# Kernel tuning notes

Hardware: AMD Instinct MI355X
Metric: run time of the kernel (lower is better)

## Reference

```python
import jax, jax.numpy as jnp
import numpy as np

HEADS = 8
DIM = 64      # dim
DH = 64       # dim_head
DK = 24       # dim_k (== dim_head_k * heads, required by reshape in forward)
DHK = 3       # dim_head_k (also conv groups)


def setup_inputs() -> dict:
    key = jax.random.key(0)
    ks = jax.random.split(key, 10)
    b, h, w = 4, 128, 128
    return {
        "x_in": jax.random.normal(ks[0], (b, h, w, DIM), jnp.float32),
        "illu_fea_trans": jax.random.normal(ks[1], (b, h, w, DIM), jnp.float32),
        "illu_map_trans": jax.random.normal(ks[2], (b, h, w, DK), jnp.float32),
        # Linear weights stored as [in, out] (torch stores [out, in]; math y = x @ W_in_out)
        "Wq": jax.random.normal(ks[3], (DIM, HEADS * DH), jnp.float32) * 0.05,
        "Wk": jax.random.normal(ks[4], (DK, HEADS * DHK), jnp.float32) * 0.05,
        "Wv": jax.random.normal(ks[5], (DIM, HEADS * DH), jnp.float32) * 0.05,
        "rescale": jnp.ones((HEADS, 1, 1), jnp.float32),
        "Wp": jax.random.normal(ks[6], (HEADS * DHK, DK), jnp.float32) * 0.05,
        "bp": jax.random.normal(ks[7], (DK,), jnp.float32) * 0.05,
        # grouped conv weights, OIHW: [out=24, in/groups=8, 3, 3]
        "conv1_w": jax.random.normal(ks[8], (DK, DK // DHK, 3, 3), jnp.float32) * 0.05,
        "conv2_w": jax.random.normal(ks[9], (DK, DK // DHK, 3, 3), jnp.float32) * 0.05,
    }


def _gconv(x_nchw, w_oihw):
    return jax.lax.conv_general_dilated(
        x_nchw, w_oihw, window_strides=(1, 1), padding='SAME',
        feature_group_count=DHK,
        dimension_numbers=('NCHW', 'OIHW', 'NCHW'))


def reference(x_in, illu_fea_trans, illu_map_trans, Wq, Wk, Wv, rescale, Wp, bp, conv1_w, conv2_w):
    b, h, w, c = x_in.shape
    n = h * w
    # projections
    q = (x_in.reshape(b, n, c) @ Wq).reshape(b, n, HEADS, DH)
    k_inp = illu_map_trans.reshape(b, n, DK) @ Wk            # [b, n, heads*dhk]
    v = (illu_fea_trans.reshape(b, n, c) @ Wv).reshape(b, n, HEADS, DH)
    kh = k_inp.reshape(b, n, HEADS, DHK)
    q = q / (DIM ** 0.5)  # note: scaled by sqrt(dim), not sqrt(dim_head)
    # channel-wise cross-attention: attn over channel dims, contracting tokens n
    attn = jnp.einsum('bnhk,bnhd->bhkd', kh, q) * rescale[None]  # [b, heads, dhk, dh]
    attn = jax.nn.softmax(attn, axis=-1)
    out = jnp.einsum('bhkd,bnhd->bnkh', attn, v)             # [b, n, dhk, heads]
    out = out.reshape(b, n, DHK * HEADS) @ Wp + bp           # proj
    out = out.reshape(b, h, w, DK)
    # positional branch: two grouped 3x3 convs with exact GELU on k_inp
    kx = k_inp.reshape(b, h, w, DK).transpose(0, 3, 1, 2)    # NCHW
    y = _gconv(kx, conv1_w)
    y = jax.nn.gelu(y, approximate=False)
    y = _gconv(y, conv2_w)
    return out + y.transpose(0, 2, 3, 1)
```

## Files before the change

kernel.cpp:

```cpp
#include <hip/hip_runtime.h>
#include <math.h>

#define HEADS 8
#define DIM   64
#define DK    24
#define DHK   3
#define BB    4
#define HH    128
#define WW    128
#define NN    (HH*WW)
#define QSCALE 0.125f

__global__ __launch_bounds__(1024) void s_reduce(
    const float* __restrict__ imap,
    const float* __restrict__ x,
    float* __restrict__ Sp_part,
    float* __restrict__ Pt)
{
    __shared__ float part[16 * 1540];
    const int tid = threadIdx.x;
    const int blk = blockIdx.x;
    const int b = blk >> 6, chunk = blk & 63;
    const int w = tid >> 6, lane = tid & 63;
    const int cq = lane & 15;
    const int ig = lane >> 4;

    const long tok0 = (long)b * NN + chunk * 256 + w * 16;
    const float* xp = x    + tok0 * 64 + cq * 4;
    const float* mp = imap + tok0 * 24 + ig * 6;

    float acc[6][4];
    #pragma unroll
    for (int r = 0; r < 6; ++r)
        #pragma unroll
        for (int q = 0; q < 4; ++q) acc[r][q] = 0.f;

    #pragma unroll 4
    for (int t = 0; t < 16; ++t) {
        float4 xv = *(const float4*)(xp + t * 64);
        float2 m0 = *(const float2*)(mp + t * 24);
        float2 m1 = *(const float2*)(mp + t * 24 + 2);
        float2 m2 = *(const float2*)(mp + t * 24 + 4);
        float mm[6] = {m0.x, m0.y, m1.x, m1.y, m2.x, m2.y};
        #pragma unroll
        for (int r = 0; r < 6; ++r) {
            acc[r][0] += mm[r] * xv.x;
            acc[r][1] += mm[r] * xv.y;
            acc[r][2] += mm[r] * xv.z;
            acc[r][3] += mm[r] * xv.w;
        }
    }

    float* pp = part + w * 1540;
    #pragma unroll
    for (int r = 0; r < 6; ++r) {
        float4 v = {acc[r][0], acc[r][1], acc[r][2], acc[r][3]};
        *(float4*)(pp + (ig * 6 + r) * 64 + cq * 4) = v;
    }
    __syncthreads();

    for (int e = tid; e < 1536; e += 1024) {
        float s = 0.f;
        #pragma unroll
        for (int ww = 0; ww < 16; ++ww) s += part[ww * 1540 + e];
        Sp_part[(long)blk * 1536 + e] = s;
    }
    if (blk < 4)
        for (int e = tid; e < 1536; e += 1024) Pt[blk * 1536 + e] = 0.f;
}

__global__ __launch_bounds__(256) void attn_fused(
    const float* __restrict__ Sp_part,
    const float* __restrict__ Wk,
    const float* __restrict__ Wq,
    const float* __restrict__ Wv,
    const float* __restrict__ rescale,
    const float* __restrict__ Wp,
    float* __restrict__ Pt)
{
    __shared__ float Sp_l[1536];
    __shared__ float sS[192];
    __shared__ float sP[192];
    __shared__ float Wv_l[64 * 65];

    const int tid = threadIdx.x, blk = blockIdx.x;
    const int b = blk >> 3, h = blk & 7;
    const int w = tid >> 6, lane = tid & 63;

    {
        float s[6] = {0.f, 0.f, 0.f, 0.f, 0.f, 0.f};
        const float* p = Sp_part + (long)(b * 64) * 1536 + tid;
        #pragma unroll 8
        for (int pb = 0; pb < 64; ++pb)
            #pragma unroll
            for (int k = 0; k < 6; ++k)
                s[k] += p[(long)pb * 1536 + k * 256];
        #pragma unroll
        for (int k = 0; k < 6; ++k) Sp_l[tid + k * 256] = s[k];
    }
    for (int e = tid; e < 4096; e += 256) {
        int c = e >> 6, d = e & 63;
        Wv_l[c * 65 + d] = Wv[c * 512 + h * 64 + d];
    }
    __syncthreads();

    if (w < 3) {
        const float* wk = Wk + (h * 3 + w);
        float s = 0.f;
        #pragma unroll
        for (int i = 0; i < 24; ++i) s += wk[i * 24] * Sp_l[i * 64 + lane];
        sS[w * 64 + lane] = s;
    }
    __syncthreads();

    if (w < 3) {
        const float* wq = Wq + h * 64 + lane;
        const float* sr = sS + w * 64;
        float a = 0.f;
        #pragma unroll 8
        for (int c = 0; c < 64; ++c) a += sr[c] * wq[c * 512];
        a *= QSCALE * rescale[h];
        float mx = a;
        #pragma unroll
        for (int off = 32; off >= 1; off >>= 1)
            mx = fmaxf(mx, __shfl_xor(mx, off, 64));
        float e = expf(a - mx);
        float sum = e;
        #pragma unroll
        for (int off = 32; off >= 1; off >>= 1)
            sum += __shfl_xor(sum, off, 64);
        sP[w * 64 + lane] = e / sum;
    }
    __syncthreads();

    if (w < 3) {
        const float* pr = sP + w * 64;
        const float* wv = Wv_l + lane * 65;
        float m = 0.f;
        #pragma unroll
        for (int d = 0; d < 64; ++d) m += pr[d] * wv[d];
        sS[w * 64 + lane] = m;
    }
    __syncthreads();

    for (int q = tid; q < 1536; q += 256) {
        int o = q >> 6, c = q & 63;
        float v = 0.f;
        #pragma unroll
        for (int k = 0; k < 3; ++k)
            v += sS[k * 64 + c] * Wp[(k * 8 + h) * 24 + o];
        atomicAdd(&Pt[b * 1536 + o * 64 + c], v);
    }
}

__global__ __launch_bounds__(192, 2) void conv_fused(
    const float* __restrict__ imap, const float* __restrict__ Wk,
    const float* __restrict__ c1w,  const float* __restrict__ fea,
    const float* __restrict__ c2w,  const float* __restrict__ Pt,
    const float* __restrict__ bp,   float* __restrict__ outp)
{
    __shared__ __align__(16) float smem[8784];
    float* kbuf = smem;
    float* feat = smem;
    float* y1l  = smem + 4352;
    float* ptl  = smem + 7152;

    const int tid = threadIdx.x;
    const int blk = blockIdx.x;
    const int b = blk >> 8, ti = (blk >> 4) & 15, tj = blk & 15;
    const int i0 = ti * 8, j0 = tj * 8;
    const int o = tid % 24, jj = tid / 24;
    const int g = o >> 3;

    if (tid < 144) {
        const int pi = tid / 12, pj = tid % 12;
        const int gi = i0 + pi - 2, gj = j0 + pj - 2;
        float kv[24];
        #pragma unroll
        for (int j = 0; j < 24; ++j) kv[j] = 0.f;
        if (gi >= 0 && gi < HH && gj >= 0 && gj < WW) {
            const float4* m4 = (const float4*)(imap + (((long)b * HH + gi) * WW + gj) * 24);
            float m[24];
            #pragma unroll
            for (int i = 0; i < 6; ++i) {
                float4 v = m4[i];
                m[4*i+0]=v.x; m[4*i+1]=v.y; m[4*i+2]=v.z; m[4*i+3]=v.w;
            }
            for (int i = 0; i < 24; ++i) {
                float mi = m[i];
                #pragma unroll
                for (int j = 0; j < 24; ++j) kv[j] += mi * Wk[i * 24 + j];
            }
        }
        #pragma unroll
        for (int j = 0; j < 24; ++j) kbuf[tid * 28 + j] = kv[j];
    }
    __syncthreads();

    {
        float wr[8][9];
        {
            const float4* wp = (const float4*)(c1w + o * 72);
            #pragma unroll
            for (int t = 0; t < 18; ++t) ((float4*)wr)[t] = wp[t];
        }
        for (int task = tid; task < 240; task += 192) {
            const int r = task / 24;
            float wc[3][3][8];
            #pragma unroll
            for (int slot = 0; slot < 2; ++slot)
                #pragma unroll
                for (int di = 0; di < 3; ++di) {
                    const float* p = kbuf + ((r + di) * 12 + slot) * 28 + g * 8;
                    *(float4*)&wc[slot][di][0] = *(const float4*)(p);
                    *(float4*)&wc[slot][di][4] = *(const float4*)(p + 4);
                }
            #pragma unroll
            for (int c = 0; c < 10; ++c) {
                const int s2 = (c + 2) % 3;
                #pragma unroll
                for (int di = 0; di < 3; ++di) {
                    const float* p = kbuf + ((r + di) * 12 + (c + 2)) * 28 + g * 8;
                    *(float4*)&wc[s2][di][0] = *(const float4*)(p);
                    *(float4*)&wc[s2][di][4] = *(const float4*)(p + 4);
                }
                float s = 0.f;
                #pragma unroll
                for (int dj = 0; dj < 3; ++dj) {
                    const int sl = (c + dj) % 3;
                    #pragma unroll
                    for (int di = 0; di < 3; ++di)
                        #pragma unroll
                        for (int ic = 0; ic < 8; ++ic)
                            s += wc[sl][di][ic] * wr[ic][di * 3 + dj];
                }
                const int gi = i0 + r - 1, gj = j0 + c - 1;
                float val = 0.f;
                if (gi >= 0 && gi < HH && gj >= 0 && gj < WW)
                    val = 0.5f * s * (1.f + erff(s * 0.70710678f));
                y1l[(r * 10 + c) * 28 + o] = val;
            }
        }
    }
    __syncthreads();

    {
        const float4* feaT4 = (const float4*)(fea + (((long)(b * HH + i0)) * WW + j0) * 64);
        float4* feat4 = (float4*)feat;
        for (int e = tid; e < 1024; e += 192) {
            const int pix = e >> 4, cq = e & 15;
            feat4[pix * 17 + cq] =
                feaT4[((long)(pix >> 3) * WW + (pix & 7)) * 16 + cq];
        }
        const float4* Pt4 = (const float4*)(Pt + b * 1536);
        float4* ptl4 = (float4*)ptl;
        for (int e = tid; e < 384; e += 192) {
            const int o2 = e >> 4, cq = e & 15;
            ptl4[o2 * 17 + cq] = Pt4[o2 * 16 + cq];
        }
    }
    __syncthreads();

    float wr[8][9];
    {
        const float4* wp = (const float4*)(c2w + o * 72);
        #pragma unroll
        for (int t = 0; t < 18; ++t) ((float4*)wr)[t] = wp[t];
    }

    float acc[8];
    {
        const float bo = bp[o];
        #pragma unroll
        for (int ii = 0; ii < 8; ++ii) acc[ii] = bo;
        const float4* pr4 = (const float4*)(ptl + o * 68);
        for (int cq = 0; cq < 16; ++cq) {
            float4 p = pr4[cq];
            #pragma unroll
            for (int ii = 0; ii < 8; ++ii) {
                float4 f = ((const float4*)(feat + (ii * 8 + jj) * 68))[cq];
                acc[ii] += f.x * p.x + f.y * p.y + f.z * p.z + f.w * p.w;
            }
        }
    }

    float win[3][3][8];
    #define LROW(R, SLOT)                                                     \
    {                                                                         \
        const float* rp_ = y1l + ((R) * 10 + jj) * 28 + g * 8;                \
        *(float4*)&win[SLOT][0][0] = *(const float4*)(rp_);                   \
        *(float4*)&win[SLOT][0][4] = *(const float4*)(rp_ + 4);               \
        *(float4*)&win[SLOT][1][0] = *(const float4*)(rp_ + 28);              \
        *(float4*)&win[SLOT][1][4] = *(const float4*)(rp_ + 32);              \
        *(float4*)&win[SLOT][2][0] = *(const float4*)(rp_ + 56);              \
        *(float4*)&win[SLOT][2][4] = *(const float4*)(rp_ + 60);              \
    }

    LROW(0, 0)
    LROW(1, 1)
    #pragma unroll
    for (int ii = 0; ii < 8; ++ii) {
        LROW(ii + 2, (ii + 2) % 3)
        float s = 0.f;
        #pragma unroll
        for (int di = 0; di < 3; ++di) {
            const int slot = (ii + di) % 3;
            #pragma unroll
            for (int dj = 0; dj < 3; ++dj)
                #pragma unroll
                for (int ic = 0; ic < 8; ++ic)
                    s += win[slot][dj][ic] * wr[ic][di * 3 + dj];
        }
        outp[((long)((b * HH + i0 + ii) * WW + j0)) * 24 + tid] = acc[ii] + s;
    }
    #undef LROW
}

extern "C" void kernel_launch(void* const* d_in, const int* in_sizes, int n_in,
                              void* d_out, int out_size, void* d_ws, size_t ws_size,
                              hipStream_t stream) {
    const float* x_in    = (const float*)d_in[0];
    const float* fea     = (const float*)d_in[1];
    const float* imap    = (const float*)d_in[2];
    const float* Wq      = (const float*)d_in[3];
    const float* Wk      = (const float*)d_in[4];
    const float* Wv      = (const float*)d_in[5];
    const float* rescale = (const float*)d_in[6];
    const float* Wp      = (const float*)d_in[7];
    const float* bp      = (const float*)d_in[8];
    const float* c1w     = (const float*)d_in[9];
    const float* c2w     = (const float*)d_in[10];
    float* out = (float*)d_out;

    float* ws      = (float*)d_ws;
    float* Sp_part = ws;
    float* Pt      = ws + 393216;

    s_reduce<<<256, 1024, 0, stream>>>(imap, x_in, Sp_part, Pt);
    attn_fused<<<32, 256, 0, stream>>>(Sp_part, Wk, Wq, Wv, rescale, Wp, Pt);
    conv_fused<<<BB * 256, 192, 0, stream>>>(imap, Wk, c1w, fea, c2w, Pt, bp, out);
}
```

Before: 152.4 us.

## Rebalance token reduction into smaller blocks and fuse per-head attention into one block per batch

The token reduction now uses 1024 blocks of 256 threads, each covering 64 tokens, in place of 256 blocks of 1024 threads, which spreads the reduction across more workgroups. The attention stage now runs one 1024-thread block per batch covering all heads, in place of 8 head blocks per batch. This removes the Pt zeroing and the atomicAdd accumulation. The trade-off is that the attention stage reads four times as many partial sums across only 4 blocks, so its serial reduction of 256 partial sums per batch may take longer.

```diff
diff --git a/kernel.cpp b/kernel.cpp
--- a/kernel.cpp
+++ b/kernel.cpp
@@ -11,21 +11,20 @@
 #define NN    (HH*WW)
 #define QSCALE 0.125f
 
-__global__ __launch_bounds__(1024) void s_reduce(
+__global__ __launch_bounds__(256) void s_reduce(
     const float* __restrict__ imap,
     const float* __restrict__ x,
-    float* __restrict__ Sp_part,
-    float* __restrict__ Pt)
+    float* __restrict__ Sp_part)
 {
-    __shared__ float part[16 * 1540];
+    __shared__ float part[4 * 1540];
     const int tid = threadIdx.x;
     const int blk = blockIdx.x;
-    const int b = blk >> 6, chunk = blk & 63;
+    const int b = blk >> 8, chunk = blk & 255;
     const int w = tid >> 6, lane = tid & 63;
     const int cq = lane & 15;
     const int ig = lane >> 4;
 
-    const long tok0 = (long)b * NN + chunk * 256 + w * 16;
+    const long tok0 = (long)b * NN + chunk * 64 + w * 16;
     const float* xp = x    + tok0 * 64 + cq * 4;
     const float* mp = imap + tok0 * 24 + ig * 6;
 
@@ -59,17 +58,13 @@
     }
     __syncthreads();
 
-    for (int e = tid; e < 1536; e += 1024) {
-        float s = 0.f;
-        #pragma unroll
-        for (int ww = 0; ww < 16; ++ww) s += part[ww * 1540 + e];
-        Sp_part[(long)blk * 1536 + e] = s;
-    }
-    if (blk < 4)
-        for (int e = tid; e < 1536; e += 1024) Pt[blk * 1536 + e] = 0.f;
+    for (int e = tid; e < 1536; e += 256) {
+        Sp_part[(long)blk * 1536 + e] =
+            part[e] + part[1540 + e] + part[3080 + e] + part[4620 + e];
+    }
 }
 
-__global__ __launch_bounds__(256) void attn_fused(
+__global__ __launch_bounds__(1024) void attn_fused(
     const float* __restrict__ Sp_part,
     const float* __restrict__ Wk,
     const float* __restrict__ Wq,
@@ -78,78 +73,91 @@
     const float* __restrict__ Wp,
     float* __restrict__ Pt)
 {
+    __shared__ float part[4 * 1536];
     __shared__ float Sp_l[1536];
-    __shared__ float sS[192];
-    __shared__ float sP[192];
-    __shared__ float Wv_l[64 * 65];
-
-    const int tid = threadIdx.x, blk = blockIdx.x;
-    const int b = blk >> 3, h = blk & 7;
+    __shared__ float S_l[1536];
+    __shared__ float att[1536];
+
+    const int tid = threadIdx.x, b = blockIdx.x;
     const int w = tid >> 6, lane = tid & 63;
 
     {
-        float s[6] = {0.f, 0.f, 0.f, 0.f, 0.f, 0.f};
-        const float* p = Sp_part + (long)(b * 64) * 1536 + tid;
+        const int p = tid & 255, q = tid >> 8;
+        const float* base = Sp_part + ((long)(b * 256 + q * 64)) * 1536;
+        #pragma unroll
+        for (int k = 0; k < 6; ++k) {
+            const int e = k * 256 + p;
+            const float* pp = base + e;
+            float s = 0.f;
+            #pragma unroll 16
+            for (int sb = 0; sb < 64; ++sb) s += pp[(long)sb * 1536];
+            part[q * 1536 + e] = s;
+        }
+    }
+    __syncthreads();
+    for (int e = tid; e < 1536; e += 1024)
+        Sp_l[e] = part[e] + part[1536 + e] + part[3072 + e] + part[4608 + e];
+    __syncthreads();
+
+    for (int e = tid; e < 1536; e += 1024) {
+        const int c = e & 63, ch = e >> 6;
+        float s = 0.f;
+        #pragma unroll
+        for (int i = 0; i < 24; ++i) s += Wk[i * 24 + ch] * Sp_l[i * 64 + c];
+        S_l[e] = s;
+    }
+    __syncthreads();
+
+    for (int e = tid; e < 1536; e += 1024) {
+        const int d = e & 63, ch = e >> 6, h = ch / 3;
+        const float* wq = Wq + h * 64 + d;
+        const float* sr = S_l + ch * 64;
+        float s = 0.f;
         #pragma unroll 8
-        for (int pb = 0; pb < 64; ++pb)
-            #pragma unroll
-            for (int k = 0; k < 6; ++k)
-                s[k] += p[(long)pb * 1536 + k * 256];
-        #pragma unroll
-        for (int k = 0; k < 6; ++k) Sp_l[tid + k * 256] = s[k];
-    }
-    for (int e = tid; e < 4096; e += 256) {
-        int c = e >> 6, d = e & 63;
-        Wv_l[c * 65 + d] = Wv[c * 512 + h * 64 + d];
-    }
-    __syncthreads();
-
-    if (w < 3) {
-        const float* wk = Wk + (h * 3 + w);
-        float s = 0.f;
-        #pragma unroll
-        for (int i = 0; i < 24; ++i) s += wk[i * 24] * Sp_l[i * 64 + lane];
-        sS[w * 64 + lane] = s;
-    }
-    __syncthreads();
-
-    if (w < 3) {
-        const float* wq = Wq + h * 64 + lane;
-        const float* sr = sS + w * 64;
-        float a = 0.f;
-        #pragma unroll 8
-        for (int c = 0; c < 64; ++c) a += sr[c] * wq[c * 512];
-        a *= QSCALE * rescale[h];
-        float mx = a;
-        #pragma unroll
-        for (int off = 32; off >= 1; off >>= 1)
-            mx = fmaxf(mx, __shfl_xor(mx, off, 64));
-        float e = expf(a - mx);
-        float sum = e;
-        #pragma unroll
-        for (int off = 32; off >= 1; off >>= 1)
-            sum += __shfl_xor(sum, off, 64);
-        sP[w * 64 + lane] = e / sum;
-    }
-    __syncthreads();
-
-    if (w < 3) {
-        const float* pr = sP + w * 64;
-        const float* wv = Wv_l + lane * 65;
-        float m = 0.f;
-        #pragma unroll
-        for (int d = 0; d < 64; ++d) m += pr[d] * wv[d];
-        sS[w * 64 + lane] = m;
-    }
-    __syncthreads();
-
-    for (int q = tid; q < 1536; q += 256) {
-        int o = q >> 6, c = q & 63;
-        float v = 0.f;
+        for (int c = 0; c < 64; ++c) s += sr[c] * wq[c * 512];
+        att[e] = s * QSCALE * rescale[h];
+    }
+    __syncthreads();
+
+    #pragma unroll
+    for (int pass = 0; pass < 2; ++pass) {
+        const int r = w + pass * 16;
+        if (r < 24 && (pass == 0 || w < 8)) {
+            float a = att[r * 64 + lane];
+            float mx = a;
+            #pragma unroll
+            for (int off = 32; off >= 1; off >>= 1)
+                mx = fmaxf(mx, __shfl_xor(mx, off, 64));
+            float e = expf(a - mx);
+            float sum = e;
+            #pragma unroll
+            for (int off = 32; off >= 1; off >>= 1)
+                sum += __shfl_xor(sum, off, 64);
+            att[r * 64 + lane] = e / sum;
+        }
+    }
+    __syncthreads();
+
+    for (int e = tid; e < 1536; e += 1024) {
+        const int c = e & 63, ch = e >> 6, h = ch / 3;
+        const float* pr = att + ch * 64;
+        const float* wv = Wv + c * 512 + h * 64;
+        float s = 0.f;
+        #pragma unroll
+        for (int d = 0; d < 64; ++d) s += pr[d] * wv[d];
+        S_l[e] = s;
+    }
+    __syncthreads();
+
+    for (int e = tid; e < 1536; e += 1024) {
+        const int c = e & 63, o = e >> 6;
+        float s = 0.f;
         #pragma unroll
         for (int k = 0; k < 3; ++k)
-            v += sS[k * 64 + c] * Wp[(k * 8 + h) * 24 + o];
-        atomicAdd(&Pt[b * 1536 + o * 64 + c], v);
+            #pragma unroll
+            for (int h = 0; h < 8; ++h)
+                s += S_l[(h * 3 + k) * 64 + c] * Wp[(k * 8 + h) * 24 + o];
+        Pt[b * 1536 + e] = s;
     }
 }
 
@@ -334,9 +342,9 @@
 
     float* ws      = (float*)d_ws;
     float* Sp_part = ws;
-    float* Pt      = ws + 393216;
-
-    s_reduce<<<256, 1024, 0, stream>>>(imap, x_in, Sp_part, Pt);
-    attn_fused<<<32, 256, 0, stream>>>(Sp_part, Wk, Wq, Wv, rescale, Wp, Pt);
+    float* Pt      = ws + 1572864;
+
+    s_reduce<<<1024, 256, 0, stream>>>(imap, x_in, Sp_part);
+    attn_fused<<<4, 1024, 0, stream>>>(Sp_part, Wk, Wq, Wv, rescale, Wp, Pt);
     conv_fused<<<BB * 256, 192, 0, stream>>>(imap, Wk, c1w, fea, c2w, Pt, bp, out);
 }
```

Result: slower. 179.0 us (+17.4%).
